# Kernel tuning notes

Measured on AMD Instinct MI355X. Metric: run time of the kernel, lower is better.

The kernel has to match this reference:

```python
import math
import jax, jax.numpy as jnp
import numpy as np

B, S, D_MODEL, NUM_HEADS = 4, 2048, 1024, 16
D_N = D_MODEL // NUM_HEADS  # 64


def setup_inputs() -> dict:
    key = jax.random.key(0)
    ks = jax.random.split(key, 10)
    scale = 1.0 / math.sqrt(D_MODEL)
    return {
        "q": jax.random.normal(ks[0], (B, S, D_MODEL), dtype=jnp.float32),
        "k": jax.random.normal(ks[1], (B, S, D_MODEL), dtype=jnp.float32),
        "v": jax.random.normal(ks[2], (B, S, D_MODEL), dtype=jnp.float32),
        "mask": jax.random.uniform(ks[3], (B, S, S), dtype=jnp.float32),
        "w_q": jax.random.normal(ks[4], (D_N, D_MODEL), dtype=jnp.float32) * scale,
        "b_q": jnp.zeros((D_N,), dtype=jnp.float32),
        "w_k": jax.random.normal(ks[5], (D_N, D_MODEL), dtype=jnp.float32) * scale,
        "b_k": jnp.zeros((D_N,), dtype=jnp.float32),
        "w_v": jax.random.normal(ks[6], (D_N, D_MODEL), dtype=jnp.float32) * scale,
        "b_v": jnp.zeros((D_N,), dtype=jnp.float32),
    }


def reference(q, k, v, mask, w_q, b_q, w_k, b_k, w_v, b_v):
    # Linear projections d_model -> d_n (torch Linear: x @ W.T + b)
    qp = jnp.einsum("bsd,nd->bsn", q, w_q) + b_q  # [B,S,d_n]
    kp = jnp.einsum("bsd,nd->bsn", k, w_k) + b_k
    vp = jnp.einsum("bsd,nd->bsn", v, w_v) + b_v
    # Scaled dot-product scores with additive mask penalty
    scores = jnp.einsum("bqn,bkn->bqk", qp, kp) / math.sqrt(D_N) + mask * (-1e9)
    attn = jax.nn.softmax(scores, axis=-1)  # [B,S,S]
    return jnp.einsum("bqk,bkn->bqn", attn, vp)  # [B,S,d_n]
```

## Files before the change

kernel.cpp:

```cpp
#include <hip/hip_runtime.h>
#include <hip/hip_bf16.h>

#define BB 4
#define SS 2048
#define DM 1024
#define DN 64

typedef short short8 __attribute__((ext_vector_type(8)));
typedef float f32x4 __attribute__((ext_vector_type(4)));
typedef unsigned short ushort;

__device__ __forceinline__ ushort f2bf(float f) {
    union { float f; unsigned u; } v; v.f = f;
    unsigned r = v.u + 0x7fffu + ((v.u >> 16) & 1u);
    return (ushort)(r >> 16);
}

__global__ __launch_bounds__(256) void prep_w(
    const float* __restrict__ wq, const float* __restrict__ wk,
    const float* __restrict__ wv, ushort* __restrict__ w_bf)
{
    int i = blockIdx.x * 256 + threadIdx.x;
    int p = i >> 14;
    int j = (i & 16383) * 4;
    const float* src = (p == 0) ? wq : (p == 1) ? wk : wv;
    float4 f = *(const float4*)(src + j);
    ushort o[4] = { f2bf(f.x), f2bf(f.y), f2bf(f.z), f2bf(f.w) };
    *(unsigned long long*)(w_bf + p * 65536 + j) = *(unsigned long long*)o;
}

__global__ __launch_bounds__(128) void proj_kernel(
    const float* __restrict__ q, const float* __restrict__ k, const float* __restrict__ v,
    const ushort* __restrict__ w_bf,
    const float* __restrict__ bq, const float* __restrict__ bk, const float* __restrict__ bvp,
    ushort* __restrict__ qp, ushort* __restrict__ kp, ushort* __restrict__ vpT)
{
    const int tid  = threadIdx.x;
    const int proj = blockIdx.y;
    const int wv_id = tid >> 6;
    const int lane  = tid & 63;
    const int l16   = lane & 15;
    const int quad  = lane >> 4;
    const int g     = blockIdx.x * 2 + wv_id;
    const int m0    = g * 16;

    const float* x     = (proj == 0) ? q  : (proj == 1) ? k  : v;
    const ushort* wb   = w_bf + proj * 65536;
    const float* bias  = (proj == 0) ? bq : (proj == 1) ? bk : bvp;

    const float* arow = x + (size_t)(m0 + l16) * DM + quad * 8;

    f32x4 acc[4];
#pragma unroll
    for (int t = 0; t < 4; t++) acc[t] = (f32x4){0.f, 0.f, 0.f, 0.f};

#pragma unroll 2
    for (int kb = 0; kb < DM; kb += 32) {
        float4 f0 = *(const float4*)(arow + kb);
        float4 f1 = *(const float4*)(arow + kb + 4);
        ushort ta[8] = { f2bf(f0.x), f2bf(f0.y), f2bf(f0.z), f2bf(f0.w),
                         f2bf(f1.x), f2bf(f1.y), f2bf(f1.z), f2bf(f1.w) };
        short8 a = *(short8*)ta;
#pragma unroll
        for (int t = 0; t < 4; t++) {
            short8 b = *(const short8*)(wb + (size_t)(t * 16 + l16) * DM + kb + quad * 8);
            acc[t] = __builtin_amdgcn_mfma_f32_16x16x32_bf16(a, b, acc[t], 0, 0, 0);
        }
    }

#pragma unroll
    for (int t = 0; t < 4; t++) {
        int n = t * 16 + l16;
        float bb_ = bias[n];
#pragma unroll
        for (int r = 0; r < 4; r++) {
            int grow = m0 + quad * 4 + r;
            ushort h = f2bf(acc[t][r] + bb_);
            if (proj == 0)      qp[(size_t)grow * DN + n] = h;
            else if (proj == 1) kp[(size_t)grow * DN + n] = h;
            else {
                int bb = grow >> 11, s = grow & 2047;
                vpT[((size_t)bb * DN + n) * SS + s] = h;
            }
        }
    }
}

__global__ __launch_bounds__(256, 4) void flash_kernel(
    const float* __restrict__ mask,
    const ushort* __restrict__ qp,
    const ushort* __restrict__ kp,
    const ushort* __restrict__ vpT,
    float* __restrict__ part_O,
    float* __restrict__ part_ml,
    int nslice, int keys_per_slice)
{
    __shared__ __align__(16) ushort p_lds[4][16][80];

    const int tid  = threadIdx.x;
    const int wv   = tid >> 6;
    const int lane = tid & 63;
    const int l16  = lane & 15;
    const int quad = lane >> 4;

    const int gw     = blockIdx.x * 4 + wv;
    const int qg     = gw & 127;
    const int rest   = gw >> 7;
    const int slice  = rest % nslice;
    const int b      = rest / nslice;

    const ushort* qbase = qp + ((size_t)b * SS + qg * 16 + l16) * DN + quad * 8;
    short8 aq0 = *(const short8*)(qbase);
    short8 aq1 = *(const short8*)(qbase + 32);

    float m_r[4] = { -__builtin_inff(), -__builtin_inff(),
                     -__builtin_inff(), -__builtin_inff() };
    float l_r[4] = { 0.f, 0.f, 0.f, 0.f };
    f32x4 Oacc[4];
#pragma unroll
    for (int t = 0; t < 4; t++) Oacc[t] = (f32x4){0.f, 0.f, 0.f, 0.f};

    const size_t mrow0 = ((size_t)b * SS + qg * 16 + quad * 4) * SS;
    const int k_begin = slice * keys_per_slice;
    const int k_end   = k_begin + keys_per_slice;

    for (int k0 = k_begin; k0 < k_end; k0 += 64) {
        float mk[4][4];
#pragma unroll
        for (int t = 0; t < 4; t++)
#pragma unroll
            for (int r = 0; r < 4; r++)
                mk[t][r] = mask[mrow0 + (size_t)r * SS + k0 + t * 16 + l16];

        f32x4 sc[4];
#pragma unroll
        for (int t = 0; t < 4; t++) {
            const ushort* kb_ = kp + ((size_t)b * SS + k0 + t * 16 + l16) * DN + quad * 8;
            short8 bk0 = *(const short8*)(kb_);
            short8 bk1 = *(const short8*)(kb_ + 32);
            f32x4 z = (f32x4){0.f, 0.f, 0.f, 0.f};
            z = __builtin_amdgcn_mfma_f32_16x16x32_bf16(aq0, bk0, z, 0, 0, 0);
            z = __builtin_amdgcn_mfma_f32_16x16x32_bf16(aq1, bk1, z, 0, 0, 0);
            sc[t] = z;
        }

#pragma unroll
        for (int r = 0; r < 4; r++) {
            float s[4];
            float tmax = -__builtin_inff();
#pragma unroll
            for (int t = 0; t < 4; t++) {
                s[t] = sc[t][r] * 0.125f - 1e9f * mk[t][r];
                tmax = fmaxf(tmax, s[t]);
            }
#pragma unroll
            for (int off = 8; off >= 1; off >>= 1)
                tmax = fmaxf(tmax, __shfl_xor(tmax, off, 16));
            float mnew  = fmaxf(m_r[r], tmax);
            float alpha = __expf(m_r[r] - mnew);
            m_r[r] = mnew;
            float rs = 0.f;
#pragma unroll
            for (int t = 0; t < 4; t++) {
                float pv = __expf(s[t] - mnew);
                rs += pv;
                p_lds[wv][quad * 4 + r][t * 16 + l16] = f2bf(pv);
            }
#pragma unroll
            for (int off = 8; off >= 1; off >>= 1)
                rs += __shfl_xor(rs, off, 16);
            l_r[r] = l_r[r] * alpha + rs;
#pragma unroll
            for (int tf = 0; tf < 4; tf++)
                Oacc[tf][r] *= alpha;
        }

        short8 ap0 = *(const short8*)&p_lds[wv][l16][quad * 8];
        short8 ap1 = *(const short8*)&p_lds[wv][l16][32 + quad * 8];
#pragma unroll
        for (int tf = 0; tf < 4; tf++) {
            const ushort* vb_ = vpT + ((size_t)b * DN + tf * 16 + l16) * SS + k0 + quad * 8;
            short8 bv0 = *(const short8*)(vb_);
            short8 bv1 = *(const short8*)(vb_ + 32);
            Oacc[tf] = __builtin_amdgcn_mfma_f32_16x16x32_bf16(ap0, bv0, Oacc[tf], 0, 0, 0);
            Oacc[tf] = __builtin_amdgcn_mfma_f32_16x16x32_bf16(ap1, bv1, Oacc[tf], 0, 0, 0);
        }
    }

    const int rowg = (b * SS + qg * 16) + quad * 4;
#pragma unroll
    for (int r = 0; r < 4; r++) {
        size_t row = (size_t)rowg + r;
        if (l16 == 0) {
            part_ml[((size_t)slice * (BB * SS) + row) * 2 + 0] = m_r[r];
            part_ml[((size_t)slice * (BB * SS) + row) * 2 + 1] = l_r[r];
        }
#pragma unroll
        for (int tf = 0; tf < 4; tf++)
            part_O[((size_t)slice * (BB * SS) + row) * DN + tf * 16 + l16] = Oacc[tf][r];
    }
}

__global__ __launch_bounds__(256) void combine_kernel(
    const float* __restrict__ part_O, const float* __restrict__ part_ml,
    float* __restrict__ out, int nslice)
{
    const int tid = threadIdx.x;
    const int row = blockIdx.x * 4 + (tid >> 6);
    const int f   = tid & 63;

    float ms[8], ls[8];
    float M = -__builtin_inff();
    for (int i = 0; i < nslice; i++) {
        ms[i] = part_ml[((size_t)i * (BB * SS) + row) * 2 + 0];
        ls[i] = part_ml[((size_t)i * (BB * SS) + row) * 2 + 1];
        M = fmaxf(M, ms[i]);
    }
    float L = 0.f, acc = 0.f;
    for (int i = 0; i < nslice; i++) {
        float e = __expf(ms[i] - M);
        L += e * ls[i];
        acc += e * part_O[((size_t)i * (BB * SS) + row) * DN + f];
    }
    out[(size_t)row * DN + f] = acc / L;
}

extern "C" void kernel_launch(void* const* d_in, const int* in_sizes, int n_in,
                              void* d_out, int out_size, void* d_ws, size_t ws_size,
                              hipStream_t stream) {
    const float* q    = (const float*)d_in[0];
    const float* k    = (const float*)d_in[1];
    const float* v    = (const float*)d_in[2];
    const float* mask = (const float*)d_in[3];
    const float* wq   = (const float*)d_in[4];
    const float* bq   = (const float*)d_in[5];
    const float* wk   = (const float*)d_in[6];
    const float* bk   = (const float*)d_in[7];
    const float* wv   = (const float*)d_in[8];
    const float* bv   = (const float*)d_in[9];
    float* out = (float*)d_out;

    char* p = (char*)d_ws;
    ushort* w_bf = (ushort*)p;                 p += 3 * 65536 * sizeof(ushort);
    ushort* qp   = (ushort*)p;                 p += (size_t)BB * SS * DN * 2;
    ushort* kp   = (ushort*)p;                 p += (size_t)BB * SS * DN * 2;
    ushort* vpT  = (ushort*)p;                 p += (size_t)BB * SS * DN * 2;
    size_t fixed = (size_t)(p - (char*)d_ws);

    int split = 8;
    while (split > 1 &&
           fixed + (size_t)split * ((size_t)BB * SS * 2 * 4 + (size_t)BB * SS * DN * 4) > ws_size)
        split >>= 1;

    float* part_ml = (float*)p;                p += (size_t)split * BB * SS * 2 * 4;
    float* part_O  = (float*)p;

    int keys_per_slice = SS / split;

    prep_w<<<192, 256, 0, stream>>>(wq, wk, wv, w_bf);
    proj_kernel<<<dim3(256, 3), 128, 0, stream>>>(q, k, v, w_bf, bq, bk, bv, qp, kp, vpT);
    flash_kernel<<<128 * split, 256, 0, stream>>>(mask, qp, kp, vpT, part_O, part_ml,
                                                  split, keys_per_slice);
    combine_kernel<<<(BB * SS) / 4, 256, 0, stream>>>(part_O, part_ml, out, split);
}
```

Measured before the change: 227.7 us.

## Split projection K-dimension across four waves with LDS reduction

```diff
diff --git a/kernel.cpp b/kernel.cpp
--- a/kernel.cpp
+++ b/kernel.cpp
@@ -29,33 +29,34 @@
     *(unsigned long long*)(w_bf + p * 65536 + j) = *(unsigned long long*)o;
 }
 
-__global__ __launch_bounds__(128) void proj_kernel(
+__global__ __launch_bounds__(256, 6) void proj_kernel(
     const float* __restrict__ q, const float* __restrict__ k, const float* __restrict__ v,
     const ushort* __restrict__ w_bf,
     const float* __restrict__ bq, const float* __restrict__ bk, const float* __restrict__ bvp,
     ushort* __restrict__ qp, ushort* __restrict__ kp, ushort* __restrict__ vpT)
 {
+    __shared__ __align__(16) float red[4][16][65];
+
     const int tid  = threadIdx.x;
-    const int proj = blockIdx.y;
     const int wv_id = tid >> 6;
     const int lane  = tid & 63;
     const int l16   = lane & 15;
     const int quad  = lane >> 4;
-    const int g     = blockIdx.x * 2 + wv_id;
-    const int m0    = g * 16;
+    const int proj  = blockIdx.y;
+    const int m0    = blockIdx.x * 16;
 
     const float* x     = (proj == 0) ? q  : (proj == 1) ? k  : v;
     const ushort* wb   = w_bf + proj * 65536;
-    const float* bias  = (proj == 0) ? bq : (proj == 1) ? bk : bvp;
 
     const float* arow = x + (size_t)(m0 + l16) * DM + quad * 8;
+    const int kb0 = wv_id << 8;
 
     f32x4 acc[4];
 #pragma unroll
     for (int t = 0; t < 4; t++) acc[t] = (f32x4){0.f, 0.f, 0.f, 0.f};
 
 #pragma unroll 2
-    for (int kb = 0; kb < DM; kb += 32) {
+    for (int kb = kb0; kb < kb0 + 256; kb += 32) {
         float4 f0 = *(const float4*)(arow + kb);
         float4 f1 = *(const float4*)(arow + kb + 4);
         ushort ta[8] = { f2bf(f0.x), f2bf(f0.y), f2bf(f0.z), f2bf(f0.w),
@@ -69,19 +70,28 @@
     }
 
 #pragma unroll
-    for (int t = 0; t < 4; t++) {
-        int n = t * 16 + l16;
-        float bb_ = bias[n];
-#pragma unroll
-        for (int r = 0; r < 4; r++) {
-            int grow = m0 + quad * 4 + r;
-            ushort h = f2bf(acc[t][r] + bb_);
-            if (proj == 0)      qp[(size_t)grow * DN + n] = h;
-            else if (proj == 1) kp[(size_t)grow * DN + n] = h;
-            else {
-                int bb = grow >> 11, s = grow & 2047;
-                vpT[((size_t)bb * DN + n) * SS + s] = h;
-            }
+    for (int t = 0; t < 4; t++)
+#pragma unroll
+        for (int r = 0; r < 4; r++)
+            red[wv_id][quad * 4 + r][t * 16 + l16] = acc[t][r];
+    __syncthreads();
+
+    const float* bias = (proj == 0) ? bq : (proj == 1) ? bk : bvp;
+    const int col   = tid & 63;
+    const int rbase = tid >> 6;
+    const float bb_ = bias[col];
+#pragma unroll
+    for (int rr = 0; rr < 4; rr++) {
+        const int row = rr * 4 + rbase;
+        float s_ = red[0][row][col] + red[1][row][col]
+                 + red[2][row][col] + red[3][row][col];
+        ushort h = f2bf(s_ + bb_);
+        int grow = m0 + row;
+        if (proj == 0)      qp[(size_t)grow * DN + col] = h;
+        else if (proj == 1) kp[(size_t)grow * DN + col] = h;
+        else {
+            int bb = grow >> 11, s = grow & 2047;
+            vpT[((size_t)bb * DN + col) * SS + s] = h;
         }
     }
 }
@@ -258,7 +268,7 @@
     int keys_per_slice = SS / split;
 
     prep_w<<<192, 256, 0, stream>>>(wq, wk, wv, w_bf);
-    proj_kernel<<<dim3(256, 3), 128, 0, stream>>>(q, k, v, w_bf, bq, bk, bv, qp, kp, vpT);
+    proj_kernel<<<dim3(512, 3), 256, 0, stream>>>(q, k, v, w_bf, bq, bk, bv, qp, kp, vpT);
     flash_kernel<<<128 * split, 256, 0, stream>>>(mask, qp, kp, vpT, part_O, part_ml,
                                                   split, keys_per_slice);
     combine_kernel<<<(BB * SS) / 4, 256, 0, stream>>>(part_O, part_ml, out, split);
```

New measurement: 234.1 us. 1.03x slower.

## Stage projection input tiles through double-buffered LDS with coalesced row loads

Applied to the files above, without the earlier changes.

```diff
diff --git a/kernel.cpp b/kernel.cpp
--- a/kernel.cpp
+++ b/kernel.cpp
@@ -35,46 +35,74 @@
     const float* __restrict__ bq, const float* __restrict__ bk, const float* __restrict__ bvp,
     ushort* __restrict__ qp, ushort* __restrict__ kp, ushort* __restrict__ vpT)
 {
+    __shared__ __align__(16) ushort sA[2][32][264];
+
     const int tid  = threadIdx.x;
-    const int proj = blockIdx.y;
     const int wv_id = tid >> 6;
     const int lane  = tid & 63;
     const int l16   = lane & 15;
     const int quad  = lane >> 4;
-    const int g     = blockIdx.x * 2 + wv_id;
-    const int m0    = g * 16;
-
-    const float* x     = (proj == 0) ? q  : (proj == 1) ? k  : v;
-    const ushort* wb   = w_bf + proj * 65536;
-    const float* bias  = (proj == 0) ? bq : (proj == 1) ? bk : bvp;
-
-    const float* arow = x + (size_t)(m0 + l16) * DM + quad * 8;
+    const int proj  = blockIdx.y;
+    const int m0    = blockIdx.x * 32;
+
+    const float* x   = (proj == 0) ? q  : (proj == 1) ? k  : v;
+    const ushort* wb = w_bf + proj * 65536;
 
     f32x4 acc[4];
 #pragma unroll
     for (int t = 0; t < 4; t++) acc[t] = (f32x4){0.f, 0.f, 0.f, 0.f};
 
-#pragma unroll 2
-    for (int kb = 0; kb < DM; kb += 32) {
-        float4 f0 = *(const float4*)(arow + kb);
-        float4 f1 = *(const float4*)(arow + kb + 4);
-        ushort ta[8] = { f2bf(f0.x), f2bf(f0.y), f2bf(f0.z), f2bf(f0.w),
-                         f2bf(f1.x), f2bf(f1.y), f2bf(f1.z), f2bf(f1.w) };
-        short8 a = *(short8*)ta;
-#pragma unroll
-        for (int t = 0; t < 4; t++) {
-            short8 b = *(const short8*)(wb + (size_t)(t * 16 + l16) * DM + kb + quad * 8);
-            acc[t] = __builtin_amdgcn_mfma_f32_16x16x32_bf16(a, b, acc[t], 0, 0, 0);
-        }
-    }
-
+    float4 st[16];
+
+#pragma unroll
+    for (int it = 0; it < 16; it++)
+        st[it] = *(const float4*)(x + (size_t)(m0 + 2 * it + wv_id) * DM + lane * 4);
+#pragma unroll
+    for (int it = 0; it < 16; it++) {
+        ushort o[4] = { f2bf(st[it].x), f2bf(st[it].y), f2bf(st[it].z), f2bf(st[it].w) };
+        *(unsigned long long*)&sA[0][2 * it + wv_id][lane * 4] = *(unsigned long long*)o;
+    }
+    __syncthreads();
+
+#pragma unroll
+    for (int c = 0; c < 4; c++) {
+        const int cur = c & 1;
+        if (c < 3) {
+#pragma unroll
+            for (int it = 0; it < 16; it++)
+                st[it] = *(const float4*)(x + (size_t)(m0 + 2 * it + wv_id) * DM
+                                            + (c + 1) * 256 + lane * 4);
+        }
+#pragma unroll
+        for (int s = 0; s < 8; s++) {
+            const int kbL = s * 32;
+            short8 a = *(const short8*)&sA[cur][wv_id * 16 + l16][kbL + quad * 8];
+#pragma unroll
+            for (int t = 0; t < 4; t++) {
+                short8 b = *(const short8*)(wb + (size_t)(t * 16 + l16) * DM
+                                               + c * 256 + kbL + quad * 8);
+                acc[t] = __builtin_amdgcn_mfma_f32_16x16x32_bf16(a, b, acc[t], 0, 0, 0);
+            }
+        }
+        if (c < 3) {
+#pragma unroll
+            for (int it = 0; it < 16; it++) {
+                ushort o[4] = { f2bf(st[it].x), f2bf(st[it].y), f2bf(st[it].z), f2bf(st[it].w) };
+                *(unsigned long long*)&sA[cur ^ 1][2 * it + wv_id][lane * 4] =
+                    *(unsigned long long*)o;
+            }
+        }
+        __syncthreads();
+    }
+
+    const float* bias = (proj == 0) ? bq : (proj == 1) ? bk : bvp;
 #pragma unroll
     for (int t = 0; t < 4; t++) {
         int n = t * 16 + l16;
         float bb_ = bias[n];
 #pragma unroll
         for (int r = 0; r < 4; r++) {
-            int grow = m0 + quad * 4 + r;
+            int grow = m0 + wv_id * 16 + quad * 4 + r;
             ushort h = f2bf(acc[t][r] + bb_);
             if (proj == 0)      qp[(size_t)grow * DN + n] = h;
             else if (proj == 1) kp[(size_t)grow * DN + n] = h;
```

New measurement: 232.0 us. No clear change (+1.9%).

## Stage projection activations through LDS with async double-buffered global_load_lds

Applied to the files above, without the earlier changes.

```diff
diff --git a/kernel.cpp b/kernel.cpp
--- a/kernel.cpp
+++ b/kernel.cpp
@@ -14,6 +14,12 @@
     union { float f; unsigned u; } v; v.f = f;
     unsigned r = v.u + 0x7fffu + ((v.u >> 16) & 1u);
     return (ushort)(r >> 16);
+}
+
+__device__ __forceinline__ void gll16(const void* g, void* l) {
+    __builtin_amdgcn_global_load_lds(
+        (const __attribute__((address_space(1))) void*)g,
+        (__attribute__((address_space(3))) void*)l, 16, 0, 0);
 }
 
 __global__ __launch_bounds__(256) void prep_w(
@@ -29,45 +35,71 @@
     *(unsigned long long*)(w_bf + p * 65536 + j) = *(unsigned long long*)o;
 }
 
-__global__ __launch_bounds__(128) void proj_kernel(
+__global__ __launch_bounds__(64) void proj_kernel(
     const float* __restrict__ q, const float* __restrict__ k, const float* __restrict__ v,
     const ushort* __restrict__ w_bf,
     const float* __restrict__ bq, const float* __restrict__ bk, const float* __restrict__ bvp,
     ushort* __restrict__ qp, ushort* __restrict__ kp, ushort* __restrict__ vpT)
 {
-    const int tid  = threadIdx.x;
+    __shared__ __align__(16) float sA[2][16][256];
+
+    const int lane = threadIdx.x;
+    const int l16  = lane & 15;
+    const int quad = lane >> 4;
     const int proj = blockIdx.y;
-    const int wv_id = tid >> 6;
-    const int lane  = tid & 63;
-    const int l16   = lane & 15;
-    const int quad  = lane >> 4;
-    const int g     = blockIdx.x * 2 + wv_id;
-    const int m0    = g * 16;
-
-    const float* x     = (proj == 0) ? q  : (proj == 1) ? k  : v;
-    const ushort* wb   = w_bf + proj * 65536;
-    const float* bias  = (proj == 0) ? bq : (proj == 1) ? bk : bvp;
-
-    const float* arow = x + (size_t)(m0 + l16) * DM + quad * 8;
+    const int m0   = blockIdx.x * 16;
+
+    const float* x   = (proj == 0) ? q  : (proj == 1) ? k  : v;
+    const ushort* wb = w_bf + proj * 65536;
+
+    const int swz  = lane * 16;
+    const int swzr = (l16 & 7) << 4;
 
     f32x4 acc[4];
 #pragma unroll
     for (int t = 0; t < 4; t++) acc[t] = (f32x4){0.f, 0.f, 0.f, 0.f};
 
-#pragma unroll 2
-    for (int kb = 0; kb < DM; kb += 32) {
-        float4 f0 = *(const float4*)(arow + kb);
-        float4 f1 = *(const float4*)(arow + kb + 4);
-        ushort ta[8] = { f2bf(f0.x), f2bf(f0.y), f2bf(f0.z), f2bf(f0.w),
-                         f2bf(f1.x), f2bf(f1.y), f2bf(f1.z), f2bf(f1.w) };
-        short8 a = *(short8*)ta;
-#pragma unroll
-        for (int t = 0; t < 4; t++) {
-            short8 b = *(const short8*)(wb + (size_t)(t * 16 + l16) * DM + kb + quad * 8);
-            acc[t] = __builtin_amdgcn_mfma_f32_16x16x32_bf16(a, b, acc[t], 0, 0, 0);
-        }
-    }
-
+#define STAGE(c_, b_)                                                         \
+    {                                                                         \
+        const char* gx = (const char*)x + (size_t)m0 * 4096 + (size_t)(c_) * 1024; \
+        _Pragma("unroll")                                                     \
+        for (int j = 0; j < 16; j++)                                          \
+            gll16(gx + (size_t)j * 4096 + (swz ^ ((j & 7) << 4)),             \
+                  &sA[b_][j][0]);                                             \
+    }
+
+    STAGE(0, 0);
+
+#pragma unroll
+    for (int c = 0; c < 4; c++) {
+        const int cur = c & 1;
+        if (c < 3) STAGE(c + 1, cur ^ 1);
+        __builtin_amdgcn_sched_barrier(0);
+        if (c < 3) { asm volatile("s_waitcnt vmcnt(16)" ::: "memory"); }
+        else       { asm volatile("s_waitcnt vmcnt(0)"  ::: "memory"); }
+        __builtin_amdgcn_sched_barrier(0);
+
+#pragma unroll
+        for (int s = 0; s < 8; s++) {
+            const char* rb = (const char*)&sA[cur][l16][0];
+            const int o = s * 128 + quad * 32;
+            f32x4 fa0 = *(const f32x4*)(rb + ((o)      ^ swzr));
+            f32x4 fa1 = *(const f32x4*)(rb + ((o + 16) ^ swzr));
+            ushort ta[8] = { f2bf(fa0[0]), f2bf(fa0[1]), f2bf(fa0[2]), f2bf(fa0[3]),
+                             f2bf(fa1[0]), f2bf(fa1[1]), f2bf(fa1[2]), f2bf(fa1[3]) };
+            short8 a = *(short8*)ta;
+            const int kglob = c * 256 + s * 32;
+#pragma unroll
+            for (int t = 0; t < 4; t++) {
+                short8 b = *(const short8*)(wb + (size_t)(t * 16 + l16) * DM
+                                               + kglob + quad * 8);
+                acc[t] = __builtin_amdgcn_mfma_f32_16x16x32_bf16(a, b, acc[t], 0, 0, 0);
+            }
+        }
+    }
+#undef STAGE
+
+    const float* bias = (proj == 0) ? bq : (proj == 1) ? bk : bvp;
 #pragma unroll
     for (int t = 0; t < 4; t++) {
         int n = t * 16 + l16;
@@ -258,7 +290,7 @@
     int keys_per_slice = SS / split;
 
     prep_w<<<192, 256, 0, stream>>>(wq, wk, wv, w_bf);
-    proj_kernel<<<dim3(256, 3), 128, 0, stream>>>(q, k, v, w_bf, bq, bk, bv, qp, kp, vpT);
+    proj_kernel<<<dim3(512, 3), 64, 0, stream>>>(q, k, v, w_bf, bq, bk, bv, qp, kp, vpT);
     flash_kernel<<<128 * split, 256, 0, stream>>>(mask, qp, kp, vpT, part_O, part_ml,
                                                   split, keys_per_slice);
     combine_kernel<<<(BB * SS) / 4, 256, 0, stream>>>(part_O, part_ml, out, split);
```

Result: slower. 245.8 us (+8.0%).
